# Kernel optimization log

Hardware: AMD Instinct MI355X
Metric: run time of the kernel (lower is better)

Reference implementation:

```python
import jax, jax.numpy as jnp
import numpy as np

LN_EPS = 1e-5  # torch nn.LayerNorm default


def setup_inputs() -> dict:
    key = jax.random.key(0)
    kx, kw = jax.random.split(key)
    tokens, d_in, d_out = 8192, 4096, 16384
    x = jax.random.normal(kx, (tokens, d_in), dtype=jnp.float32)
    # nn.Linear weight layout: [out_features, in_features]
    W = jax.random.normal(kw, (d_out, d_in), dtype=jnp.float32) * (1.0 / np.sqrt(d_in))
    return {"x": x, "W": W}


def reference(x, W):
    # LayerNorm over last dim, no affine params (elementwise_affine=False)
    mean = jnp.mean(x, axis=-1, keepdims=True)
    var = jnp.mean(jnp.square(x - mean), axis=-1, keepdims=True)  # biased, as torch LN
    xn = (x - mean) * jax.lax.rsqrt(var + LN_EPS)
    # Linear (no bias): [tokens, d_in] @ [d_in, d_out]
    y = jnp.einsum("td,od->to", xn, W)
    return jax.nn.sigmoid(y)
```

## Files before the change

### kernel.cpp

```cpp
#include <hip/hip_runtime.h>
#include <hip/hip_bf16.h>
#include <stdint.h>

#define TOKENS 8192
#define DIN    4096
#define DOUT   16384

#define BM 256
#define BN 256
#define BKT 64
#define NT (DIN / BKT)
#define NJ (NT / 2)

typedef short s16x8 __attribute__((ext_vector_type(8)));
typedef float f32x4 __attribute__((ext_vector_type(4)));

#define AS1 __attribute__((address_space(1)))
#define AS3 __attribute__((address_space(3)))
#define VMCNT(n)  asm volatile("s_waitcnt vmcnt(" #n ")" ::: "memory")
#define LGKM0()   asm volatile("s_waitcnt lgkmcnt(0)" ::: "memory")
#define LGKM8()   asm volatile("s_waitcnt lgkmcnt(8)" ::: "memory")
#define SCHEDB()  __builtin_amdgcn_sched_barrier(0)
#define BAR()     __builtin_amdgcn_s_barrier()
#define PRIO1()   __builtin_amdgcn_s_setprio(1)
#define PRIO0()   __builtin_amdgcn_s_setprio(0)

__device__ __forceinline__ unsigned short f2bf(float f) {
  unsigned int u = __float_as_uint(f);
  u += 0x7fffu + ((u >> 16) & 1u);
  return (unsigned short)(u >> 16);
}

__global__ __launch_bounds__(256) void ln_kernel(const float* __restrict__ x,
                                                 unsigned short* __restrict__ xn) {
  const int row = blockIdx.x;
  const float4* xr = reinterpret_cast<const float4*>(x + (size_t)row * DIN);
  float4 v[4];
  float sum = 0.f, ssq = 0.f;
#pragma unroll
  for (int i = 0; i < 4; ++i) {
    v[i] = xr[threadIdx.x + i * 256];
    sum += v[i].x + v[i].y + v[i].z + v[i].w;
    ssq += v[i].x * v[i].x + v[i].y * v[i].y + v[i].z * v[i].z + v[i].w * v[i].w;
  }
#pragma unroll
  for (int off = 32; off > 0; off >>= 1) {
    sum += __shfl_xor(sum, off, 64);
    ssq += __shfl_xor(ssq, off, 64);
  }
  __shared__ float red[8];
  const int wid = threadIdx.x >> 6;
  if ((threadIdx.x & 63) == 0) { red[wid] = sum; red[wid + 4] = ssq; }
  __syncthreads();
  sum = red[0] + red[1] + red[2] + red[3];
  ssq = red[4] + red[5] + red[6] + red[7];
  const float mean = sum * (1.f / DIN);
  const float var  = ssq * (1.f / DIN) - mean * mean;
  const float rs   = rsqrtf(var + 1e-5f);
  ushort4* xo = reinterpret_cast<ushort4*>(xn + (size_t)row * DIN);
#pragma unroll
  for (int i = 0; i < 4; ++i) {
    ushort4 o;
    o.x = f2bf((v[i].x - mean) * rs);
    o.y = f2bf((v[i].y - mean) * rs);
    o.z = f2bf((v[i].z - mean) * rs);
    o.w = f2bf((v[i].w - mean) * rs);
    xo[threadIdx.x + i * 256] = o;
  }
}

__global__ __launch_bounds__(256) void cvt_kernel(const float* __restrict__ W,
                                                  unsigned short* __restrict__ Wb) {
  const size_t i = (size_t)blockIdx.x * 256 + threadIdx.x;
  float4 v = reinterpret_cast<const float4*>(W)[i];
  ushort4 o;
  o.x = f2bf(v.x); o.y = f2bf(v.y); o.z = f2bf(v.z); o.w = f2bf(v.w);
  reinterpret_cast<ushort4*>(Wb)[i] = o;
}

__global__ __launch_bounds__(512, 2) void gemm_sig(const unsigned short* __restrict__ A,
                                                   const unsigned short* __restrict__ B,
                                                   float* __restrict__ C) {
  __shared__ unsigned short Asl[2 * 256 * 64];
  __shared__ unsigned short Bsl[2 * 256 * 64];

  const int bid = blockIdx.x;
  const int cpx = gridDim.x >> 3;
  const int swz = (bid & 7) * cpx + (bid >> 3);
  const int bm = swz & 31;
  const int bn = swz >> 5;

  const int tid  = threadIdx.x;
  const int wid  = tid >> 6;
  const int lane = tid & 63;
  const int wr = wid >> 2, wc = wid & 3;

  const unsigned short* gA = A + (size_t)bm * BM * DIN;
  const unsigned short* gB = B + (size_t)bn * BN * DIN;

  const int l8 = lane >> 3, l7 = lane & 7;
  const int csw = l7 ^ l8;
  const unsigned short* sA = gA + (size_t)(wid * 8 + l8) * DIN + csw * 8;
  const unsigned short* sB = gB + (size_t)(wid * 8 + l8) * DIN + csw * 8;
  const int dOfs = wid * 512;

#define STG_Aq(p, q, kt) __builtin_amdgcn_global_load_lds( \
    (const AS1 void*)(sA + (size_t)(q) * 64 * DIN + (size_t)(kt) * BKT), \
    (AS3 void*)(Asl + ((p) * 256 + (q) * 64) * 64 + dOfs), 16, 0, 0)
#define STG_Bq(p, q, kt) __builtin_amdgcn_global_load_lds( \
    (const AS1 void*)(sB + (size_t)(q) * 64 * DIN + (size_t)(kt) * BKT), \
    (AS3 void*)(Bsl + ((p) * 256 + (q) * 64) * 64 + dOfs), 16, 0, 0)

  int aO[8], bO[4];
#pragma unroll
  for (int m = 0; m < 8; ++m) aO[m] = (wr * 128 + m * 16 + (lane & 15)) * 64;
#pragma unroll
  for (int n = 0; n < 4; ++n) bO[n] = (wc * 64 + n * 16 + (lane & 15)) * 64;
  const int slt0 = ((lane >> 4) ^ l7) * 8;
  const int slt1 = (((lane >> 4) + 4) ^ l7) * 8;

  s16x8 a0[4], a1[4], b0k0[2], b0k1[2], b1k0[2], b1k1[2];
  f32x4 acc[8][4] = {};

#define RD_A2(p, mb4) do { _Pragma("unroll") for (int mm = 0; mm < 4; ++mm) { \
    const unsigned short* _b = Asl + (p) * 16384 + aO[(mb4) + mm]; \
    a0[mm] = *reinterpret_cast<const s16x8*>(_b + slt0); \
    a1[mm] = *reinterpret_cast<const s16x8*>(_b + slt1); } } while (0)
#define RD_B2(p, nb2, d0, d1) do { _Pragma("unroll") for (int nn = 0; nn < 2; ++nn) { \
    const unsigned short* _b = Bsl + (p) * 16384 + bO[(nb2) + nn]; \
    d0[nn] = *reinterpret_cast<const s16x8*>(_b + slt0); \
    d1[nn] = *reinterpret_cast<const s16x8*>(_b + slt1); } } while (0)
#define MM8(mb4, nb2, bk0, bk1) do { _Pragma("unroll") for (int mm = 0; mm < 4; ++mm) \
    _Pragma("unroll") for (int nn = 0; nn < 2; ++nn) { \
      acc[(mb4) + mm][(nb2) + nn] = __builtin_amdgcn_mfma_f32_16x16x32_bf16(a0[mm], bk0[nn], acc[(mb4) + mm][(nb2) + nn], 0, 0, 0); \
      acc[(mb4) + mm][(nb2) + nn] = __builtin_amdgcn_mfma_f32_16x16x32_bf16(a1[mm], bk1[nn], acc[(mb4) + mm][(nb2) + nn], 0, 0, 0); } } while (0)

  STG_Aq(0, 0, 0); STG_Aq(0, 1, 0); STG_Aq(0, 2, 0); STG_Aq(0, 3, 0);
  STG_Bq(0, 0, 0); STG_Bq(0, 1, 0); STG_Bq(0, 2, 0); STG_Bq(0, 3, 0);
  STG_Aq(1, 0, 1); STG_Aq(1, 2, 1);
  STG_Bq(1, 0, 1); STG_Bq(1, 1, 1); STG_Bq(1, 2, 1); STG_Bq(1, 3, 1);
  STG_Aq(1, 1, 1); STG_Aq(1, 3, 1);
  VMCNT(8); BAR();

  for (int j = 0; j < NJ - 1; ++j) {
    const int t2 = 2 * j + 2, t3 = 2 * j + 3;
    RD_A2(0, 0); RD_B2(0, 0, b0k0, b0k1);
    LGKM8();
    BAR(); LGKM0(); SCHEDB();
    PRIO1(); MM8(0, 0, b0k0, b0k1); PRIO0(); BAR();
    RD_B2(0, 2, b1k0, b1k1);
    STG_Aq(0, 0, t2); STG_Aq(0, 2, t2);
    BAR(); LGKM0(); SCHEDB();
    PRIO1(); MM8(0, 2, b1k0, b1k1); PRIO0(); BAR();
    RD_A2(0, 4);
    STG_Bq(0, 0, t2); STG_Bq(0, 1, t2);
    BAR(); LGKM0(); SCHEDB();
    PRIO1(); MM8(4, 0, b0k0, b0k1); PRIO0(); BAR();
    VMCNT(4);
    STG_Bq(0, 2, t2); STG_Bq(0, 3, t2); STG_Aq(0, 1, t2); STG_Aq(0, 3, t2);
    BAR();
    PRIO1(); MM8(4, 2, b1k0, b1k1); PRIO0(); BAR();
    RD_A2(1, 0); RD_B2(1, 0, b0k0, b0k1);
    LGKM8();
    BAR(); LGKM0(); SCHEDB();
    PRIO1(); MM8(0, 0, b0k0, b0k1); PRIO0(); BAR();
    RD_B2(1, 2, b1k0, b1k1);
    STG_Aq(1, 0, t3); STG_Aq(1, 2, t3);
    BAR(); LGKM0(); SCHEDB();
    PRIO1(); MM8(0, 2, b1k0, b1k1); PRIO0(); BAR();
    RD_A2(1, 4);
    STG_Bq(1, 0, t3); STG_Bq(1, 1, t3);
    BAR(); LGKM0(); SCHEDB();
    PRIO1(); MM8(4, 0, b0k0, b0k1); PRIO0(); BAR();
    VMCNT(4);
    STG_Bq(1, 2, t3); STG_Bq(1, 3, t3); STG_Aq(1, 1, t3); STG_Aq(1, 3, t3);
    BAR();
    PRIO1(); MM8(4, 2, b1k0, b1k1); PRIO0(); BAR();
  }

  {
    RD_A2(0, 0); RD_B2(0, 0, b0k0, b0k1);
    LGKM8();
    BAR(); LGKM0(); SCHEDB();
    PRIO1(); MM8(0, 0, b0k0, b0k1); PRIO0(); BAR();
    RD_B2(0, 2, b1k0, b1k1);
    BAR(); LGKM0(); SCHEDB();
    PRIO1(); MM8(0, 2, b1k0, b1k1); PRIO0(); BAR();
    RD_A2(0, 4);
    BAR(); LGKM0(); SCHEDB();
    PRIO1(); MM8(4, 0, b0k0, b0k1); PRIO0(); BAR();
    VMCNT(0);
    BAR();
    PRIO1(); MM8(4, 2, b1k0, b1k1); PRIO0(); BAR();
    RD_A2(1, 0); RD_B2(1, 0, b0k0, b0k1);
    LGKM8();
    BAR(); LGKM0(); SCHEDB();
    PRIO1(); MM8(0, 0, b0k0, b0k1); PRIO0(); BAR();
    RD_B2(1, 2, b1k0, b1k1);
    BAR(); LGKM0(); SCHEDB();
    PRIO1(); MM8(0, 2, b1k0, b1k1); PRIO0(); BAR();
    RD_A2(1, 4);
    BAR(); LGKM0(); SCHEDB();
    PRIO1(); MM8(4, 0, b0k0, b0k1); PRIO0(); BAR();
    PRIO1(); MM8(4, 2, b1k0, b1k1); PRIO0();
  }

#undef STG_Aq
#undef STG_Bq
#undef RD_A2
#undef RD_B2
#undef MM8

  const int crow0 = bm * BM + wr * 128 + (lane >> 4) * 4;
  const int ccol0 = bn * BN + wc * 64 + (lane & 15);
#pragma unroll
  for (int m = 0; m < 8; ++m)
#pragma unroll
    for (int n = 0; n < 4; ++n)
#pragma unroll
      for (int jj = 0; jj < 4; ++jj) {
        const float v = acc[m][n][jj];
        C[(size_t)(crow0 + m * 16 + jj) * DOUT + (ccol0 + n * 16)] = 1.f / (1.f + __expf(-v));
      }
}

extern "C" void kernel_launch(void* const* d_in, const int* in_sizes, int n_in,
                              void* d_out, int out_size, void* d_ws, size_t ws_size,
                              hipStream_t stream) {
  const float* x = (const float*)d_in[0];
  const float* W = (const float*)d_in[1];
  float* out = (float*)d_out;

  unsigned short* xn = (unsigned short*)d_ws;
  unsigned short* Wb = xn + (size_t)TOKENS * DIN;

  ln_kernel<<<TOKENS, 256, 0, stream>>>(x, xn);
  cvt_kernel<<<((size_t)DOUT * DIN) / 1024, 256, 0, stream>>>(W, Wb);
  gemm_sig<<<(TOKENS / BM) * (DOUT / BN), 512, 0, stream>>>(xn, Wb, out);
}
```

Measured before the change: 1.372 ms.

## Drop explicit LDS waitcnts and sched barriers; remap tiles in 2x2 groups

Removes the manual lgkmcnt waits and sched_barrier fences around each MFMA phase. The compiler then inserts its own waits and can interleave LDS reads with MFMAs. The block-to-tile mapping also changes so that consecutive swizzled blocks cover 2x2 groups of output tiles, aiming for better L2 reuse of the A and B panels. The risk is that the compiler places waits less well, or reorders the reads past the barriers, which could hurt the hand-tuned pipeline.

After: 1.223 ms. -10.9%, faster.

```diff
diff --git a/kernel.cpp b/kernel.cpp
--- a/kernel.cpp
+++ b/kernel.cpp
@@ -18,9 +18,6 @@
 #define AS1 __attribute__((address_space(1)))
 #define AS3 __attribute__((address_space(3)))
 #define VMCNT(n)  asm volatile("s_waitcnt vmcnt(" #n ")" ::: "memory")
-#define LGKM0()   asm volatile("s_waitcnt lgkmcnt(0)" ::: "memory")
-#define LGKM8()   asm volatile("s_waitcnt lgkmcnt(8)" ::: "memory")
-#define SCHEDB()  __builtin_amdgcn_sched_barrier(0)
 #define BAR()     __builtin_amdgcn_s_barrier()
 #define PRIO1()   __builtin_amdgcn_s_setprio(1)
 #define PRIO0()   __builtin_amdgcn_s_setprio(0)
@@ -87,8 +84,10 @@
   const int bid = blockIdx.x;
   const int cpx = gridDim.x >> 3;
   const int swz = (bid & 7) * cpx + (bid >> 3);
-  const int bm = swz & 31;
-  const int bn = swz >> 5;
+  const int grp = swz >> 2;
+  const int sub = swz & 3;
+  const int bm = ((grp & 15) << 1) | (sub & 1);
+  const int bn = ((grp >> 4) << 1) | (sub >> 1);
 
   const int tid  = threadIdx.x;
   const int wid  = tid >> 6;
@@ -145,32 +144,30 @@
   for (int j = 0; j < NJ - 1; ++j) {
     const int t2 = 2 * j + 2, t3 = 2 * j + 3;
     RD_A2(0, 0); RD_B2(0, 0, b0k0, b0k1);
-    LGKM8();
-    BAR(); LGKM0(); SCHEDB();
+    BAR();
     PRIO1(); MM8(0, 0, b0k0, b0k1); PRIO0(); BAR();
     RD_B2(0, 2, b1k0, b1k1);
     STG_Aq(0, 0, t2); STG_Aq(0, 2, t2);
-    BAR(); LGKM0(); SCHEDB();
+    BAR();
     PRIO1(); MM8(0, 2, b1k0, b1k1); PRIO0(); BAR();
     RD_A2(0, 4);
     STG_Bq(0, 0, t2); STG_Bq(0, 1, t2);
-    BAR(); LGKM0(); SCHEDB();
+    BAR();
     PRIO1(); MM8(4, 0, b0k0, b0k1); PRIO0(); BAR();
     VMCNT(4);
     STG_Bq(0, 2, t2); STG_Bq(0, 3, t2); STG_Aq(0, 1, t2); STG_Aq(0, 3, t2);
     BAR();
     PRIO1(); MM8(4, 2, b1k0, b1k1); PRIO0(); BAR();
     RD_A2(1, 0); RD_B2(1, 0, b0k0, b0k1);
-    LGKM8();
-    BAR(); LGKM0(); SCHEDB();
+    BAR();
     PRIO1(); MM8(0, 0, b0k0, b0k1); PRIO0(); BAR();
     RD_B2(1, 2, b1k0, b1k1);
     STG_Aq(1, 0, t3); STG_Aq(1, 2, t3);
-    BAR(); LGKM0(); SCHEDB();
+    BAR();
     PRIO1(); MM8(0, 2, b1k0, b1k1); PRIO0(); BAR();
     RD_A2(1, 4);
     STG_Bq(1, 0, t3); STG_Bq(1, 1, t3);
-    BAR(); LGKM0(); SCHEDB();
+    BAR();
     PRIO1(); MM8(4, 0, b0k0, b0k1); PRIO0(); BAR();
     VMCNT(4);
     STG_Bq(1, 2, t3); STG_Bq(1, 3, t3); STG_Aq(1, 1, t3); STG_Aq(1, 3, t3);
@@ -180,27 +177,25 @@
 
   {
     RD_A2(0, 0); RD_B2(0, 0, b0k0, b0k1);
-    LGKM8();
-    BAR(); LGKM0(); SCHEDB();
+    BAR();
     PRIO1(); MM8(0, 0, b0k0, b0k1); PRIO0(); BAR();
     RD_B2(0, 2, b1k0, b1k1);
-    BAR(); LGKM0(); SCHEDB();
+    BAR();
     PRIO1(); MM8(0, 2, b1k0, b1k1); PRIO0(); BAR();
     RD_A2(0, 4);
-    BAR(); LGKM0(); SCHEDB();
+    BAR();
     PRIO1(); MM8(4, 0, b0k0, b0k1); PRIO0(); BAR();
     VMCNT(0);
     BAR();
     PRIO1(); MM8(4, 2, b1k0, b1k1); PRIO0(); BAR();
     RD_A2(1, 0); RD_B2(1, 0, b0k0, b0k1);
-    LGKM8();
-    BAR(); LGKM0(); SCHEDB();
+    BAR();
     PRIO1(); MM8(0, 0, b0k0, b0k1); PRIO0(); BAR();
     RD_B2(1, 2, b1k0, b1k1);
-    BAR(); LGKM0(); SCHEDB();
+    BAR();
     PRIO1(); MM8(0, 2, b1k0, b1k1); PRIO0(); BAR();
     RD_A2(1, 4);
-    BAR(); LGKM0(); SCHEDB();
+    BAR();
     PRIO1(); MM8(4, 0, b0k0, b0k1); PRIO0(); BAR();
     PRIO1(); MM8(4, 2, b1k0, b1k1); PRIO0();
   }
```
